# Kernel optimization log

Measured on AMD Instinct MI355X. Metric: run time of the kernel, lower is better.

## Reference

```python
import jax, jax.numpy as jnp
import numpy as np

D_MODEL = 512
N = 2048
BS = 8


def setup_inputs() -> dict:
    key = jax.random.key(0)
    ks = jax.random.split(key, 5)
    inputs1 = jax.random.normal(ks[0], (BS, N, D_MODEL), dtype=jnp.float32)
    inputs2 = jax.random.normal(ks[1], (BS, N, D_MODEL), dtype=jnp.float32)
    # torch Linear weights: init.normal_(std=0.001), bias=0
    Wq = 0.001 * jax.random.normal(ks[2], (D_MODEL, D_MODEL), dtype=jnp.float32)
    Wk = 0.001 * jax.random.normal(ks[3], (D_MODEL, D_MODEL), dtype=jnp.float32)
    Wv = 0.001 * jax.random.normal(ks[4], (D_MODEL, D_MODEL), dtype=jnp.float32)
    bq = jnp.zeros((D_MODEL,), dtype=jnp.float32)
    bk = jnp.zeros((D_MODEL,), dtype=jnp.float32)
    bv = jnp.zeros((D_MODEL,), dtype=jnp.float32)
    # nn.Parameter(torch.ones((n, n)))
    position_biases = jnp.ones((N, N), dtype=jnp.float32)
    return {"inputs1": inputs1, "inputs2": inputs2, "Wq": Wq, "bq": bq,
            "Wk": Wk, "bk": bk, "Wv": Wv, "bv": bv,
            "position_biases": position_biases}


def reference(inputs1, inputs2, Wq, bq, Wk, bk, Wv, bv, position_biases):
    # torch Linear: y = x @ W.T + b
    q = inputs1 @ Wq.T + bq                     # [b, n, d]
    k = inputs1 @ Wk.T + bk                     # [b, s, d]
    v = inputs2 @ Wv.T + bv                     # [b, s, d]
    # exp(k[b,s,d] + bias[t,s]) = exp(bias)[t,s] * exp(k)[b,s,d] -> separable,
    # avoiding the original's (n, bs, n, dim) broadcast intermediate.
    expB = jnp.exp(position_biases)             # [t, s]
    ek = jnp.exp(k)                             # [b, s, d]
    num = jnp.einsum('ts,bsd->btd', expB, ek * v)
    den = jnp.einsum('ts,bsd->btd', expB, ek)
    return jax.nn.sigmoid(q) * (num / den)      # [b, n, d]
```

## Files before the change

### kernel.cpp

```cpp
#include <hip/hip_runtime.h>

typedef float  f32x4  __attribute__((ext_vector_type(4)));
typedef __bf16 bf16x8 __attribute__((ext_vector_type(8)));
typedef __bf16 bf16x4 __attribute__((ext_vector_type(4)));

#define D_MODEL 512
#define SEQ     2048
#define BATCH   8
#define ROWS    (BATCH * SEQ)

#define ASYNC_COPY16(dst_lds, src_glb)                                          \
  __builtin_amdgcn_global_load_lds(                                             \
      (const __attribute__((address_space(1))) void*)(src_glb),                 \
      (__attribute__((address_space(3))) void*)(dst_lds), 16, 0, 0)

__global__ void cvt_all_kernel(const float* __restrict__ x1,
                               const float* __restrict__ x2,
                               const float* __restrict__ posb,
                               const float* __restrict__ Wq,
                               const float* __restrict__ Wk,
                               const float* __restrict__ Wv,
                               __bf16* __restrict__ x1b, __bf16* __restrict__ x2b,
                               __bf16* __restrict__ expBb, __bf16* __restrict__ wb)
{
  const int blk = blockIdx.x;
  if (blk < 16384) {
    const float* in = (blk < 8192) ? x1 : x2;
    __bf16* out = (blk < 8192) ? x1b : x2b;
    const int i = (blk & 8191) * 256 + threadIdx.x;
    float4 v = ((const float4*)in)[i];
    bf16x4 o = { (__bf16)v.x, (__bf16)v.y, (__bf16)v.z, (__bf16)v.w };
    ((bf16x4*)out)[i] = o;
  } else if (blk < 20480) {
    const int i = (blk - 16384) * 256 + threadIdx.x;
    float4 v = ((const float4*)posb)[i];
    bf16x4 o = { (__bf16)__expf(v.x), (__bf16)__expf(v.y),
                 (__bf16)__expf(v.z), (__bf16)__expf(v.w) };
    ((bf16x4*)expBb)[i] = o;
  } else {
    const int i = (blk - 20480) * 256 + threadIdx.x;
    const int nW4 = D_MODEL * D_MODEL / 4;
    const float* src = (i < nW4) ? Wq : (i < 2 * nW4) ? Wk : Wv;
    const int ii = i - ((i < nW4) ? 0 : (i < 2 * nW4) ? nW4 : 2 * nW4);
    float4 v = ((const float4*)src)[ii];
    bf16x4 o = { (__bf16)v.x, (__bf16)v.y, (__bf16)v.z, (__bf16)v.w };
    ((bf16x4*)wb)[i] = o;
  }
}

__global__ __launch_bounds__(256) void tri_gemm_kernel(
    const __bf16* __restrict__ x1b, const __bf16* __restrict__ x2b,
    const __bf16* __restrict__ wb,
    const float* __restrict__ bq, const float* __restrict__ bk,
    const float* __restrict__ bv,
    __bf16* __restrict__ sigq, __bf16* __restrict__ kT,
    __bf16* __restrict__ vT)
{
  __shared__ __align__(16) __bf16 As[128 * 64];
  __shared__ __align__(16) __bf16 Bs[128 * 64];

  const int K = D_MODEL;
  const int z = blockIdx.z;
  const int tid  = threadIdx.x;
  const int wave = tid >> 6;
  const int lane = tid & 63;
  const int quad = lane >> 4;
  const int l16  = lane & 15;
  const int wm   = (wave >> 1) * 64;
  const int wn   = (wave & 1) * 64;
  const int l8r = lane >> 3;
  const int scol = ((lane & 7) ^ l8r) * 8;
  const int F0 = blockIdx.y * 128;

  const __bf16* Ap = (z == 0) ? x1b
                   : (z == 1) ? (wb + (long long)D_MODEL * D_MODEL)
                              : (wb + 2LL * D_MODEL * D_MODEL);
  const __bf16* Bp = (z == 0) ? wb : (z == 1) ? x1b : x2b;

  const int srow = wave * 8 + l8r;

  const __bf16* ga[4]; const __bf16* gb[4];
  auto set_tile = [&](int t) {
    const int L0 = (blockIdx.x * 2 + t) * 128;
    const int m0 = (z == 0) ? L0 : F0;
    const int n0 = (z == 0) ? F0 : L0;
    #pragma unroll
    for (int i = 0; i < 4; ++i) {
      ga[i] = Ap + (long long)(m0 + i * 32 + srow) * K + scol;
      gb[i] = Bp + (long long)(n0 + i * 32 + srow) * K + scol;
    }
  };
  auto stage = [&](int k0) {
    #pragma unroll
    for (int i = 0; i < 4; ++i) {
      ASYNC_COPY16(As + (i * 32 + wave * 8) * 64, ga[i] + k0);
      ASYNC_COPY16(Bs + (i * 32 + wave * 8) * 64, gb[i] + k0);
    }
  };

  set_tile(0);
  stage(0);

  for (int t = 0; t < 2; ++t) {
    f32x4 acc[4][4];
    #pragma unroll
    for (int i = 0; i < 4; ++i)
      #pragma unroll
      for (int j = 0; j < 4; ++j) acc[i][j] = (f32x4){0.f, 0.f, 0.f, 0.f};

    for (int k0 = 0; k0 < K; k0 += 64) {
      __syncthreads();
      #pragma unroll
      for (int kk = 0; kk < 2; ++kk) {
        const int slot = ((quad + kk * 4) ^ (l16 & 7)) * 8;
        bf16x8 af[4], bfr[4];
        #pragma unroll
        for (int i = 0; i < 4; ++i)
          af[i] = *(const bf16x8*)&As[(wm + i * 16 + l16) * 64 + slot];
        #pragma unroll
        for (int j = 0; j < 4; ++j)
          bfr[j] = *(const bf16x8*)&Bs[(wn + j * 16 + l16) * 64 + slot];
        #pragma unroll
        for (int i = 0; i < 4; ++i)
          #pragma unroll
          for (int j = 0; j < 4; ++j)
            acc[i][j] = __builtin_amdgcn_mfma_f32_16x16x32_bf16(af[i], bfr[j],
                                                                acc[i][j], 0, 0, 0);
      }
      __syncthreads();
      if (k0 + 64 < K) {
        stage(k0 + 64);
      } else if (t == 0) {
        set_tile(1);
        stage(0);
      }
    }

    const int L0 = (blockIdx.x * 2 + t) * 128;
    if (z == 0) {
      const int m0 = L0, n0 = F0;
      #pragma unroll
      for (int j = 0; j < 4; ++j) {
        const int col = n0 + wn + j * 16 + l16;
        const float bvv = bq[col];
        #pragma unroll
        for (int i = 0; i < 4; ++i)
          #pragma unroll
          for (int r = 0; r < 4; ++r) {
            const int row = m0 + wm + i * 16 + quad * 4 + r;
            float x = acc[i][j][r] + bvv;
            sigq[(long long)row * D_MODEL + col] =
                (__bf16)(1.f / (1.f + __expf(-x)));
          }
      }
    } else {
      const int m0 = F0, n0 = L0;
      const float* bias = (z == 1) ? bk : bv;
      __bf16* outp = (z == 1) ? kT : vT;
      #pragma unroll
      for (int i = 0; i < 4; ++i) {
        #pragma unroll
        for (int r = 0; r < 4; ++r) {
          const int d = m0 + wm + i * 16 + quad * 4 + r;
          const float bvv = bias[d];
          #pragma unroll
          for (int j = 0; j < 4; ++j) {
            const int rr = n0 + wn + j * 16 + l16;
            outp[(long long)d * ROWS + rr] = (__bf16)(acc[i][j][r] + bvv);
          }
        }
      }
    }
  }
}

__global__ __launch_bounds__(256) void combine_kernel(
    const __bf16* __restrict__ kT, const __bf16* __restrict__ vT,
    __bf16* __restrict__ ekvT)
{
  const int c = blockIdx.x * 256 + threadIdx.x;
  const int d   = c >> 11;
  const int off = (c & 2047) * 8;
  const int b = off >> 11;
  const int s = off & 2047;

  bf16x8 kk = *(const bf16x8*)(kT + (long long)d * ROWS + off);
  bf16x8 vv = *(const bf16x8*)(vT + (long long)d * ROWS + off);
  bf16x8 ek, ev;
  #pragma unroll
  for (int e = 0; e < 8; ++e) {
    float ekf = __expf((float)kk[e]);
    ek[e] = (__bf16)ekf;
    ev[e] = (__bf16)(ekf * (float)vv[e]);
  }
  const int gr = ((d >> 5) << 6) + (d & 31);
  __bf16* outp = ekvT + (long long)b * (2 * D_MODEL) * SEQ + s;
  *(bf16x8*)(outp + (long long)gr * SEQ)        = ev;
  *(bf16x8*)(outp + (long long)(gr + 32) * SEQ) = ek;
}

#define EBM 256
#define EBN 256
#define EBK 64
#define ENT (SEQ / EBK)

__global__ __launch_bounds__(512) void einsum_fused_kernel(
    const __bf16* __restrict__ A, const __bf16* __restrict__ BtAll,
    const __bf16* __restrict__ sigq, float* __restrict__ out)
{
  extern __shared__ __align__(16) __bf16 smem[];

  const int b = blockIdx.z;
  const __bf16* Bt = BtAll + (long long)b * (2 * D_MODEL) * SEQ;

  const int tid  = threadIdx.x;
  const int wave = tid >> 6;
  const int lane = tid & 63;
  const int quad = lane >> 4;
  const int l16  = lane & 15;
  const int wm   = (wave >> 2) * 128;
  const int wn   = (wave & 3) * 64;
  const int m0   = blockIdx.x * EBM;
  const int n0   = blockIdx.y * EBN;
  const int l8r  = lane >> 3;
  const int scol = ((lane & 7) ^ l8r) * 8;

  const __bf16* gA = A  + (long long)(m0 + wave * 8 + l8r) * SEQ + scol;
  const __bf16* gB = Bt + (long long)(n0 + wave * 8 + l8r) * SEQ + scol;
  __bf16* lA = smem +         (wave * 8) * 64;
  __bf16* lB = smem + 32768 + (wave * 8) * 64;

  f32x4 acc[8][4];
  #pragma unroll
  for (int i = 0; i < 8; ++i)
    #pragma unroll
    for (int j = 0; j < 4; ++j) acc[i][j] = (f32x4){0.f, 0.f, 0.f, 0.f};

  auto stage = [&](int c, int k0) {
    #pragma unroll
    for (int i = 0; i < 4; ++i) {
      ASYNC_COPY16(lA + c * 16384 + i * 4096, gA + (long long)i * 64 * SEQ + k0);
      ASYNC_COPY16(lB + c * 16384 + i * 4096, gB + (long long)i * 64 * SEQ + k0);
    }
  };

  stage(0, 0);

  const int s0 = ((quad    ) ^ (l16 & 7)) * 8;
  const int s1 = ((quad + 4) ^ (l16 & 7)) * 8;

  for (int t = 0; t < ENT; ++t) {
    const int c = t & 1;
    if (t + 1 < ENT) {
      stage(c ^ 1, (t + 1) * EBK);
      asm volatile("s_waitcnt vmcnt(8)" ::: "memory");
    } else {
      asm volatile("s_waitcnt vmcnt(0)" ::: "memory");
    }
    __builtin_amdgcn_s_barrier();
    __builtin_amdgcn_sched_barrier(0);

    const __bf16* Ac = smem +         c * 16384 + (wm + l16) * 64;
    const __bf16* Bc = smem + 32768 + c * 16384 + (wn + l16) * 64;

    bf16x8 bfr[4][2];
    #pragma unroll
    for (int q = 0; q < 4; ++q) {
      if (q == 0) {
        #pragma unroll
        for (int j = 0; j < 4; ++j) {
          bfr[j][0] = *(const bf16x8*)&Bc[j * 1024 + s0];
          bfr[j][1] = *(const bf16x8*)&Bc[j * 1024 + s1];
        }
      }
      bf16x8 af[2][2];
      #pragma unroll
      for (int ii = 0; ii < 2; ++ii) {
        af[ii][0] = *(const bf16x8*)&Ac[(q * 2 + ii) * 1024 + s0];
        af[ii][1] = *(const bf16x8*)&Ac[(q * 2 + ii) * 1024 + s1];
      }
      __builtin_amdgcn_s_barrier();
      asm volatile("s_waitcnt lgkmcnt(0)" ::: "memory");
      __builtin_amdgcn_sched_barrier(0);
      __builtin_amdgcn_s_setprio(1);
      #pragma unroll
      for (int kk = 0; kk < 2; ++kk)
        #pragma unroll
        for (int ii = 0; ii < 2; ++ii)
          #pragma unroll
          for (int j = 0; j < 4; ++j)
            acc[q * 2 + ii][j] = __builtin_amdgcn_mfma_f32_16x16x32_bf16(
                af[ii][kk], bfr[j][kk], acc[q * 2 + ii][j], 0, 0, 0);
      __builtin_amdgcn_s_setprio(0);
      __builtin_amdgcn_s_barrier();
    }
  }

  const int g = (n0 + wn) >> 6;
  #pragma unroll
  for (int j = 0; j < 2; ++j) {
    const int d = g * 32 + j * 16 + l16;
    #pragma unroll
    for (int i = 0; i < 8; ++i) {
      #pragma unroll
      for (int r = 0; r < 4; ++r) {
        const int row = m0 + wm + i * 16 + quad * 4 + r;
        const long long off = ((long long)b * SEQ + row) * D_MODEL + d;
        const float num = acc[i][j][r];
        const float den = acc[i][j + 2][r];
        out[off] = (float)sigq[off] * (num / den);
      }
    }
  }
}

extern "C" void kernel_launch(void* const* d_in, const int* in_sizes, int n_in,
                              void* d_out, int out_size, void* d_ws, size_t ws_size,
                              hipStream_t stream) {
  const float* inputs1 = (const float*)d_in[0];
  const float* inputs2 = (const float*)d_in[1];
  const float* Wq = (const float*)d_in[2];
  const float* bq = (const float*)d_in[3];
  const float* Wk = (const float*)d_in[4];
  const float* bk = (const float*)d_in[5];
  const float* Wv = (const float*)d_in[6];
  const float* bv = (const float*)d_in[7];
  const float* posb = (const float*)d_in[8];
  float* out = (float*)d_out;

  char* ws = (char*)d_ws;
  const long long szX  = (long long)ROWS * D_MODEL * 2;
  const long long szW  = (long long)D_MODEL * D_MODEL * 2;
  const long long szEB = (long long)SEQ * SEQ * 2;
  const long long szT  = (long long)BATCH * 2 * D_MODEL * SEQ * 2;
  __bf16* x1b   = (__bf16*)(ws);                 ws += szX;
  __bf16* x2b   = (__bf16*)(ws);                 ws += szX;
  __bf16* wb    = (__bf16*)(ws);                 ws += 3 * szW;
  __bf16* expBb = (__bf16*)(ws);                 ws += szEB;
  __bf16* sigq  = (__bf16*)(ws);                 ws += szX;
  __bf16* kT    = (__bf16*)(ws);                 ws += szX;
  __bf16* vT    = (__bf16*)(ws);                 ws += szX;
  __bf16* ekvT  = (__bf16*)(ws);                 ws += szT;

  static bool attr_done = false;
  if (!attr_done) {
    hipFuncSetAttribute((const void*)einsum_fused_kernel,
                        hipFuncAttributeMaxDynamicSharedMemorySize, 131072);
    attr_done = true;
  }

  cvt_all_kernel<<<21248, 256, 0, stream>>>(inputs1, inputs2, posb,
                                            Wq, Wk, Wv,
                                            x1b, x2b, expBb, wb);

  {
    dim3 g(ROWS / 256, D_MODEL / 128, 3);
    tri_gemm_kernel<<<g, 256, 0, stream>>>(x1b, x2b, wb, bq, bk, bv,
                                           sigq, kT, vT);
  }

  combine_kernel<<<(D_MODEL * ROWS / 8) / 256, 256, 0, stream>>>(kT, vT, ekvT);

  {
    dim3 g(SEQ / EBM, (2 * D_MODEL) / EBN, BATCH);
    einsum_fused_kernel<<<g, 512, 131072, stream>>>(expBb, ekvT, sigq, out);
  }
}
```

Measured before the change: 261.8 us.

## Double-buffer projection GEMM and interleave async prefetch with MFMA phases

The projection GEMM goes from a single LDS buffer to ping-pong buffers, with both output tiles fused into one 16-step loop. Prefetch of the next K-slice is issued in pieces between the LDS fragment reads and the MFMA blocks, so global loads overlap compute instead of waiting behind __syncthreads. The second GEMM kernel likewise spreads its prefetch issues across the first two sub-phases rather than issuing them all up front, and now waits on vmcnt(0). The cost is double the LDS in the first kernel, which may reduce occupancy, plus more barriers per step.

```diff
diff --git a/kernel.cpp b/kernel.cpp
--- a/kernel.cpp
+++ b/kernel.cpp
@@ -56,8 +56,8 @@
     __bf16* __restrict__ sigq, __bf16* __restrict__ kT,
     __bf16* __restrict__ vT)
 {
-  __shared__ __align__(16) __bf16 As[128 * 64];
-  __shared__ __align__(16) __bf16 Bs[128 * 64];
+  __shared__ __align__(16) __bf16 As[2][128 * 64];
+  __shared__ __align__(16) __bf16 Bs[2][128 * 64];
 
   const int K = D_MODEL;
   const int z = blockIdx.z;
@@ -90,85 +90,110 @@
       gb[i] = Bp + (long long)(n0 + i * 32 + srow) * K + scol;
     }
   };
-  auto stage = [&](int k0) {
-    #pragma unroll
-    for (int i = 0; i < 4; ++i) {
-      ASYNC_COPY16(As + (i * 32 + wave * 8) * 64, ga[i] + k0);
-      ASYNC_COPY16(Bs + (i * 32 + wave * 8) * 64, gb[i] + k0);
-    }
+  auto stageA = [&](int c, int k0) {
+    #pragma unroll
+    for (int i = 0; i < 4; ++i)
+      ASYNC_COPY16(&As[c][(i * 32 + wave * 8) * 64], ga[i] + k0);
   };
+  auto stageB = [&](int c, int k0) {
+    #pragma unroll
+    for (int i = 0; i < 4; ++i)
+      ASYNC_COPY16(&Bs[c][(i * 32 + wave * 8) * 64], gb[i] + k0);
+  };
 
   set_tile(0);
-  stage(0);
-
-  for (int t = 0; t < 2; ++t) {
-    f32x4 acc[4][4];
-    #pragma unroll
-    for (int i = 0; i < 4; ++i)
-      #pragma unroll
-      for (int j = 0; j < 4; ++j) acc[i][j] = (f32x4){0.f, 0.f, 0.f, 0.f};
-
-    for (int k0 = 0; k0 < K; k0 += 64) {
-      __syncthreads();
-      #pragma unroll
-      for (int kk = 0; kk < 2; ++kk) {
-        const int slot = ((quad + kk * 4) ^ (l16 & 7)) * 8;
-        bf16x8 af[4], bfr[4];
-        #pragma unroll
-        for (int i = 0; i < 4; ++i)
-          af[i] = *(const bf16x8*)&As[(wm + i * 16 + l16) * 64 + slot];
+  stageA(0, 0);
+  stageB(0, 0);
+
+  f32x4 acc[4][4];
+  #pragma unroll
+  for (int i = 0; i < 4; ++i)
+    #pragma unroll
+    for (int j = 0; j < 4; ++j) acc[i][j] = (f32x4){0.f, 0.f, 0.f, 0.f};
+
+  for (int s = 0; s < 16; ++s) {
+    const int c = s & 1;
+    asm volatile("s_waitcnt vmcnt(0)" ::: "memory");
+    __builtin_amdgcn_s_barrier();
+    __builtin_amdgcn_sched_barrier(0);
+
+    const bool pf = (s + 1 < 16);
+    const int k1 = ((s + 1) & 7) * 64;
+
+    #pragma unroll
+    for (int kk = 0; kk < 2; ++kk) {
+      const int slot = ((quad + kk * 4) ^ (l16 & 7)) * 8;
+      bf16x8 af[4], bfr[4];
+      #pragma unroll
+      for (int i = 0; i < 4; ++i)
+        af[i] = *(const bf16x8*)&As[c][(wm + i * 16 + l16) * 64 + slot];
+      #pragma unroll
+      for (int j = 0; j < 4; ++j)
+        bfr[j] = *(const bf16x8*)&Bs[c][(wn + j * 16 + l16) * 64 + slot];
+      if (pf) {
+        if (kk == 0) {
+          if (s == 7) set_tile(1);
+          stageA(c ^ 1, k1);
+        } else {
+          stageB(c ^ 1, k1);
+        }
+      }
+      __builtin_amdgcn_s_barrier();
+      asm volatile("s_waitcnt lgkmcnt(0)" ::: "memory");
+      __builtin_amdgcn_sched_barrier(0);
+      __builtin_amdgcn_s_setprio(1);
+      #pragma unroll
+      for (int i = 0; i < 4; ++i)
         #pragma unroll
         for (int j = 0; j < 4; ++j)
-          bfr[j] = *(const bf16x8*)&Bs[(wn + j * 16 + l16) * 64 + slot];
+          acc[i][j] = __builtin_amdgcn_mfma_f32_16x16x32_bf16(af[i], bfr[j],
+                                                              acc[i][j], 0, 0, 0);
+      __builtin_amdgcn_s_setprio(0);
+      __builtin_amdgcn_s_barrier();
+    }
+
+    if ((s & 7) == 7) {
+      const int t = s >> 3;
+      const int L0 = (blockIdx.x * 2 + t) * 128;
+      if (z == 0) {
+        const int m0 = L0, n0 = F0;
+        #pragma unroll
+        for (int j = 0; j < 4; ++j) {
+          const int col = n0 + wn + j * 16 + l16;
+          const float bvv = bq[col];
+          #pragma unroll
+          for (int i = 0; i < 4; ++i)
+            #pragma unroll
+            for (int r = 0; r < 4; ++r) {
+              const int row = m0 + wm + i * 16 + quad * 4 + r;
+              float x = acc[i][j][r] + bvv;
+              sigq[(long long)row * D_MODEL + col] =
+                  (__bf16)(1.f / (1.f + __expf(-x)));
+            }
+        }
+      } else {
+        const int m0 = F0, n0 = L0;
+        const float* bias = (z == 1) ? bk : bv;
+        __bf16* outp = (z == 1) ? kT : vT;
+        #pragma unroll
+        for (int i = 0; i < 4; ++i) {
+          #pragma unroll
+          for (int r = 0; r < 4; ++r) {
+            const int d = m0 + wm + i * 16 + quad * 4 + r;
+            const float bvv = bias[d];
+            #pragma unroll
+            for (int j = 0; j < 4; ++j) {
+              const int rr = n0 + wn + j * 16 + l16;
+              outp[(long long)d * ROWS + rr] = (__bf16)(acc[i][j][r] + bvv);
+            }
+          }
+        }
+      }
+      if (s == 7) {
         #pragma unroll
         for (int i = 0; i < 4; ++i)
           #pragma unroll
-          for (int j = 0; j < 4; ++j)
-            acc[i][j] = __builtin_amdgcn_mfma_f32_16x16x32_bf16(af[i], bfr[j],
-                                                                acc[i][j], 0, 0, 0);
-      }
-      __syncthreads();
-      if (k0 + 64 < K) {
-        stage(k0 + 64);
-      } else if (t == 0) {
-        set_tile(1);
-        stage(0);
-      }
-    }
-
-    const int L0 = (blockIdx.x * 2 + t) * 128;
-    if (z == 0) {
-      const int m0 = L0, n0 = F0;
-      #pragma unroll
-      for (int j = 0; j < 4; ++j) {
-        const int col = n0 + wn + j * 16 + l16;
-        const float bvv = bq[col];
-        #pragma unroll
-        for (int i = 0; i < 4; ++i)
-          #pragma unroll
-          for (int r = 0; r < 4; ++r) {
-            const int row = m0 + wm + i * 16 + quad * 4 + r;
-            float x = acc[i][j][r] + bvv;
-            sigq[(long long)row * D_MODEL + col] =
-                (__bf16)(1.f / (1.f + __expf(-x)));
-          }
-      }
-    } else {
-      const int m0 = F0, n0 = L0;
-      const float* bias = (z == 1) ? bk : bv;
-      __bf16* outp = (z == 1) ? kT : vT;
-      #pragma unroll
-      for (int i = 0; i < 4; ++i) {
-        #pragma unroll
-        for (int r = 0; r < 4; ++r) {
-          const int d = m0 + wm + i * 16 + quad * 4 + r;
-          const float bvv = bias[d];
-          #pragma unroll
-          for (int j = 0; j < 4; ++j) {
-            const int rr = n0 + wn + j * 16 + l16;
-            outp[(long long)d * ROWS + rr] = (__bf16)(acc[i][j][r] + bvv);
-          }
-        }
+          for (int j = 0; j < 4; ++j) acc[i][j] = (f32x4){0.f, 0.f, 0.f, 0.f};
       }
     }
   }
@@ -236,32 +261,27 @@
     #pragma unroll
     for (int j = 0; j < 4; ++j) acc[i][j] = (f32x4){0.f, 0.f, 0.f, 0.f};
 
-  auto stage = [&](int c, int k0) {
-    #pragma unroll
-    for (int i = 0; i < 4; ++i) {
-      ASYNC_COPY16(lA + c * 16384 + i * 4096, gA + (long long)i * 64 * SEQ + k0);
-      ASYNC_COPY16(lB + c * 16384 + i * 4096, gB + (long long)i * 64 * SEQ + k0);
-    }
+  auto stage_pair = [&](int c, int k0, int i) {
+    ASYNC_COPY16(lA + c * 16384 + i * 4096, gA + (long long)i * 64 * SEQ + k0);
+    ASYNC_COPY16(lB + c * 16384 + i * 4096, gB + (long long)i * 64 * SEQ + k0);
   };
 
-  stage(0, 0);
+  #pragma unroll
+  for (int i = 0; i < 4; ++i) stage_pair(0, 0, i);
 
   const int s0 = ((quad    ) ^ (l16 & 7)) * 8;
   const int s1 = ((quad + 4) ^ (l16 & 7)) * 8;
 
   for (int t = 0; t < ENT; ++t) {
     const int c = t & 1;
-    if (t + 1 < ENT) {
-      stage(c ^ 1, (t + 1) * EBK);
-      asm volatile("s_waitcnt vmcnt(8)" ::: "memory");
-    } else {
-      asm volatile("s_waitcnt vmcnt(0)" ::: "memory");
-    }
+    asm volatile("s_waitcnt vmcnt(0)" ::: "memory");
     __builtin_amdgcn_s_barrier();
     __builtin_amdgcn_sched_barrier(0);
 
     const __bf16* Ac = smem +         c * 16384 + (wm + l16) * 64;
     const __bf16* Bc = smem + 32768 + c * 16384 + (wn + l16) * 64;
+    const bool pf = (t + 1 < ENT);
+    const int k1 = (t + 1) * EBK;
 
     bf16x8 bfr[4][2];
     #pragma unroll
@@ -278,6 +298,10 @@
       for (int ii = 0; ii < 2; ++ii) {
         af[ii][0] = *(const bf16x8*)&Ac[(q * 2 + ii) * 1024 + s0];
         af[ii][1] = *(const bf16x8*)&Ac[(q * 2 + ii) * 1024 + s1];
+      }
+      if (pf) {
+        if (q == 0) { stage_pair(c ^ 1, k1, 0); stage_pair(c ^ 1, k1, 1); }
+        else if (q == 1) { stage_pair(c ^ 1, k1, 2); stage_pair(c ^ 1, k1, 3); }
       }
       __builtin_amdgcn_s_barrier();
       asm volatile("s_waitcnt lgkmcnt(0)" ::: "memory");
```

Result: slower. 275.7 us (+5.3%).
